# Kernel tuning notes

Hardware: AMD Instinct MI355X
Metric: run time of the kernel (lower is better)

Reference implementation:

```python
import jax, jax.numpy as jnp
import numpy as np
from jax import lax

B, CIN, HID, T, H, W = 4, 32, 32, 31, 96, 96


def setup_inputs() -> dict:
    key = jax.random.key(0)
    k1, k2, k3 = jax.random.split(key, 3)
    inputs = jax.random.normal(k1, (B, CIN, T, H, W), dtype=jnp.float32)
    conv_w = jax.random.normal(k2, (2 * HID, CIN, 3, 3, 3), dtype=jnp.float32) * 0.05
    conv_b = jax.random.normal(k3, (2 * HID,), dtype=jnp.float32) * 0.05
    gamma = jnp.ones((1,), dtype=jnp.float32)
    return {"inputs": inputs, "conv_w": conv_w, "conv_b": conv_b, "gamma": gamma}


def reference(inputs, conv_w, conv_b, gamma):
    hid = conv_w.shape[0] // 2
    # Conv3d, 'same' padding, NCDHW layout -> gates [B, 2*hid, T, H, W]
    gates = lax.conv_general_dilated(
        inputs, conv_w, window_strides=(1, 1, 1), padding="SAME",
        dimension_numbers=("NCDHW", "OIDHW", "NCDHW"))
    gates = gates + conv_b[None, :, None, None, None]
    Z = jnp.tanh(gates[:, :hid])          # [B, hid, T, H, W]
    F = jax.nn.sigmoid(gates[:, hid:])    # [B, hid, T, H, W]

    # Gated recurrence over time (dim 2): h_t = f_t * h_{t-1} + (1 - f_t) * z_t
    Zt = jnp.moveaxis(Z, 2, 0)  # [T, B, hid, H, W]
    Ft = jnp.moveaxis(F, 2, 0)

    def step(h, zf):
        z, f = zf
        h = f * h + (1.0 - f) * z
        return h, h

    h0 = jnp.zeros_like(Zt[0])  # h=None <=> h0=0 since f*0+(1-f)*z
    _, hs = lax.scan(step, h0, (Zt, Ft))
    h_time = jnp.moveaxis(hs, 0, 2)  # [B, hid, T, H, W]

    # Per-spatial-location channel attention
    qh = jnp.transpose(h_time, (0, 3, 4, 1, 2))  # [B, H, W, C, T]
    scores = jnp.einsum("bhwct,bhwdt->bhwcd", qh, qh)  # [B, H, W, C, C]
    attn = jax.nn.softmax(scores, axis=3)  # softmax over row axis c (dim=3), as in torch
    attn = attn * (1.0 / np.sqrt(qh.shape[-2]))  # divide AFTER softmax by sqrt(C)
    ah = jnp.einsum("bhwcd,bhwdt->bhwct", attn, qh)  # [B, H, W, C, T]
    ah = jnp.transpose(ah, (0, 3, 4, 1, 2))  # [B, C, T, H, W]

    return gamma * ah + h_time
```

## Files before the change

### kernel.cpp

```cpp
#include <hip/hip_runtime.h>
#include <math.h>

#define B_ 4
#define CIN_ 32
#define HID_ 32
#define T_ 31
#define H_ 96
#define W_ 96
#define SP_ (H_*W_)

typedef _Float16 half8 __attribute__((ext_vector_type(8)));
typedef float f32x4 __attribute__((ext_vector_type(4)));
typedef float f32x16 __attribute__((ext_vector_type(16)));

static __device__ inline unsigned int packhh(float a, float b) {
  unsigned short ua = __builtin_bit_cast(unsigned short, (_Float16)a);
  unsigned short ub = __builtin_bit_cast(unsigned short, (_Float16)b);
  return (unsigned int)ua | ((unsigned int)ub << 16);
}

__global__ __launch_bounds__(256) void prep_w_kernel(
    const float* __restrict__ w, _Float16* __restrict__ wr) {
  int idx = blockIdx.x * 256 + threadIdx.x;
  if (idx >= 55296) return;
  int i = idx & 7;
  int lane = (idx >> 3) & 63;
  int rest = idx >> 9;
  int tap = rest % 27;
  int ocg = rest / 27;
  int m = lane & 15;
  int cin = (lane >> 4) * 8 + i;
  int oc = (m & 1) * 32 + ocg * 8 + (m >> 1);
  wr[idx] = (_Float16)(w[(oc * CIN_ + cin) * 27 + tap]);
}

#define PITCH 40
#define SROWS 8
#define SCOLS 18
#define SLICE_HF (SROWS * SCOLS * PITCH)

__global__ __launch_bounds__(256, 2) void conv_rec_mfma(
    const float* __restrict__ in, const _Float16* __restrict__ wr,
    const float* __restrict__ bias, unsigned int* __restrict__ gout) {
  __shared__ _Float16 in_s[4 * SLICE_HF];

  const int tid = threadIdx.x;
  const int tile = blockIdx.x;
  const int b = blockIdx.y;
  const int x0 = (tile % 6) * 16;
  const int y0 = (tile / 6) * 6;
  const int lane = tid & 63;
  const int ocg = tid >> 6;
  const int px = lane & 15;
  const int kq = lane >> 4;

  half8 wreg[27];
  {
    const _Float16* wp = wr + (size_t)ocg * 27 * 512 + lane * 8;
#pragma unroll
    for (int tap = 0; tap < 27; ++tap)
      wreg[tap] = *(const half8*)(wp + tap * 512);
  }

  const int c0 = ocg * 8 + 2 * kq;
  f32x4 bias4;
  bias4[0] = bias[c0];
  bias4[1] = bias[32 + c0];
  bias4[2] = bias[c0 + 1];
  bias4[3] = bias[32 + c0 + 1];

  const int s_xi = tid & 15;
  const int s_q  = tid >> 4;
  const int e_cin = tid & 31;
  const int e_yy  = tid >> 5;
  const int e_gy  = y0 - 1 + e_yy;
  const bool e_ok = ((unsigned)e_gy < (unsigned)H_);

  auto stage_full = [&](int ts) {
    _Float16* dst = in_s + (ts & 3) * SLICE_HF;
    const float* sb = in + ((size_t)(b * CIN_) * T_ + ts) * SP_;
#pragma unroll
    for (int k = 0; k < 16; ++k) {
      int rj = k * 16 + s_q;
      int cin = rj & 31;
      int yy = rj >> 5;
      int gy = y0 - 1 + yy;
      float v = 0.f;
      if ((unsigned)gy < (unsigned)H_)
        v = sb[(size_t)cin * (T_ * SP_) + gy * W_ + x0 + s_xi];
      dst[(yy * SCOLS + s_xi + 1) * PITCH + cin] = (_Float16)v;
    }
    float v0 = 0.f, v1 = 0.f;
    if (e_ok) {
      const float* rb = sb + (size_t)e_cin * (T_ * SP_) + e_gy * W_;
      if (x0 > 0) v0 = rb[x0 - 1];
      if (x0 + 16 < W_) v1 = rb[x0 + 16];
    }
    dst[(e_yy * SCOLS + 0) * PITCH + e_cin] = (_Float16)v0;
    dst[(e_yy * SCOLS + 17) * PITCH + e_cin] = (_Float16)v1;
  };

  {
    uint32_t* dz = (uint32_t*)(in_s + 3 * SLICE_HF);
    for (int e = tid; e < SLICE_HF / 2; e += 256) dz[e] = 0u;
  }
  stage_full(0);
  stage_full(1);
  __syncthreads();

  float h[6][2];
#pragma unroll
  for (int r = 0; r < 6; ++r) { h[r][0] = 0.f; h[r][1] = 0.f; }

  const int pr = ocg * 4 + kq;
  size_t obase = ((size_t)(b * 32 + pr) * T_) * SP_ + y0 * W_ + x0 + px;

  for (int t = 0; t < T_; ++t) {
    const int ts = t + 2;

    float sv[16], ev0 = 0.f, ev1 = 0.f;
    if (ts < T_) {
      const float* sb = in + ((size_t)(b * CIN_) * T_ + ts) * SP_;
#pragma unroll
      for (int k = 0; k < 16; ++k) {
        int rj = k * 16 + s_q;
        int cin = rj & 31;
        int yy = rj >> 5;
        int gy = y0 - 1 + yy;
        sv[k] = 0.f;
        if ((unsigned)gy < (unsigned)H_)
          sv[k] = sb[(size_t)cin * (T_ * SP_) + gy * W_ + x0 + s_xi];
      }
      if (e_ok) {
        const float* rb = sb + (size_t)e_cin * (T_ * SP_) + e_gy * W_;
        if (x0 > 0) ev0 = rb[x0 - 1];
        if (x0 + 16 < W_) ev1 = rb[x0 + 16];
      }
    }

    f32x4 acc[6];
#pragma unroll
    for (int r = 0; r < 6; ++r) acc[r] = bias4;

#pragma unroll
    for (int kd = 0; kd < 3; ++kd) {
      const _Float16* sb2 = in_s + ((t + 3 + kd) & 3) * SLICE_HF;
#pragma unroll
      for (int kw = 0; kw < 3; ++kw) {
        half8 brow[8];
#pragma unroll
        for (int rr = 0; rr < 8; ++rr)
          brow[rr] = *(const half8*)(sb2 + (rr * SCOLS + px + kw) * PITCH + kq * 8);
#pragma unroll
        for (int kh = 0; kh < 3; ++kh) {
          const int tap = kd * 9 + kh * 3 + kw;
#pragma unroll
          for (int r = 0; r < 6; ++r)
            acc[r] = __builtin_amdgcn_mfma_f32_16x16x32_f16(wreg[tap], brow[r + kh], acc[r], 0, 0, 0);
        }
      }
    }

    if (ts < T_) {
      _Float16* dst = in_s + (ts & 3) * SLICE_HF;
#pragma unroll
      for (int k = 0; k < 16; ++k) {
        int rj = k * 16 + s_q;
        int cin = rj & 31;
        int yy = rj >> 5;
        dst[(yy * SCOLS + s_xi + 1) * PITCH + cin] = (_Float16)sv[k];
      }
      dst[(e_yy * SCOLS + 0) * PITCH + e_cin] = (_Float16)ev0;
      dst[(e_yy * SCOLS + 17) * PITCH + e_cin] = (_Float16)ev1;
    } else if (ts == T_) {
      uint32_t* dz = (uint32_t*)(in_s + (ts & 3) * SLICE_HF);
      for (int e = tid; e < SLICE_HF / 2; e += 256) dz[e] = 0u;
    }

#pragma unroll
    for (int r = 0; r < 6; ++r) {
      float z0 = 1.f - 2.f / (1.f + __expf(2.f * acc[r][0]));
      float f0 = 1.f / (1.f + __expf(-acc[r][1]));
      h[r][0] = f0 * h[r][0] + (1.f - f0) * z0;
      float z1 = 1.f - 2.f / (1.f + __expf(2.f * acc[r][2]));
      float f1 = 1.f / (1.f + __expf(-acc[r][3]));
      h[r][1] = f1 * h[r][1] + (1.f - f1) * z1;
      gout[obase + r * W_] = packhh(h[r][0], h[r][1]);
    }
    obase += SP_;
    __syncthreads();
  }
}

#define APIT 40
#define PSTR 1288

__global__ __launch_bounds__(512) void attn_mfma(
    unsigned int* __restrict__ g, const float* __restrict__ gamma) {
  __shared__ _Float16 qh_s[16 * PSTR];
  __shared__ _Float16 qt_s[16 * PSTR];
  __shared__ _Float16 at_s[8 * 32 * APIT];

  const int tid = threadIdx.x;
  const int x0 = blockIdx.x * 16;
  const int y = blockIdx.y;
  const int b = blockIdx.z;
  const int lane = tid & 63;
  const int wv = tid >> 6;
  const float gm = gamma[0];

  for (int e = tid; e < 16 * 16 * 31; e += 512) {
    int xi = e & 15;
    int q = e >> 4;
    int t = q % 31;
    int pr = q / 31;
    unsigned int gw = g[((size_t)(b * 32 + pr) * T_ + t) * SP_ + y * W_ + x0 + xi];
    _Float16 h0 = __builtin_bit_cast(_Float16, (unsigned short)(gw & 0xffff));
    _Float16 h1 = __builtin_bit_cast(_Float16, (unsigned short)(gw >> 16));
    int c0 = 2 * pr;
    qh_s[xi * PSTR + c0 * APIT + t] = h0;
    qh_s[xi * PSTR + (c0 + 1) * APIT + t] = h1;
    qt_s[xi * PSTR + t * APIT + c0] = h0;
    qt_s[xi * PSTR + t * APIT + c0 + 1] = h1;
  }
  qh_s[(tid & 15) * PSTR + (tid >> 4) * APIT + 31] = (_Float16)0.f;
  __syncthreads();

  const int cd = lane & 31;
  const int hi = lane >> 5;

#pragma unroll
  for (int pp = 0; pp < 2; ++pp) {
    const int px = wv * 2 + pp;
    const _Float16* qs = qh_s + px * PSTR;
    const _Float16* qt = qt_s + px * PSTR;
    _Float16* as = at_s + wv * (32 * APIT);

    half8 q0 = *(const half8*)(qs + cd * APIT + hi * 8);
    half8 q1 = *(const half8*)(qs + cd * APIT + hi * 8 + 16);
    f32x16 S = {};
    S = __builtin_amdgcn_mfma_f32_32x32x16_f16(q0, q0, S, 0, 0, 0);
    S = __builtin_amdgcn_mfma_f32_32x32x16_f16(q1, q1, S, 0, 0, 0);

    float mx = S[0];
#pragma unroll
    for (int r = 1; r < 16; ++r) mx = fmaxf(mx, S[r]);
    mx = fmaxf(mx, __shfl_xor(mx, 32));
    float sm = 0.f;
    float ev[16];
#pragma unroll
    for (int r = 0; r < 16; ++r) { ev[r] = __expf(S[r] - mx); sm += ev[r]; }
    sm += __shfl_xor(sm, 32);
    const float sc = 0.17677669529663688f / sm;

#pragma unroll
    for (int r = 0; r < 16; ++r) {
      int c = (r & 3) + 8 * (r >> 2) + 4 * hi;
      as[c * APIT + cd] = (_Float16)(ev[r] * sc);
    }

    half8 a0 = *(const half8*)(as + cd * APIT + hi * 8);
    half8 a1 = *(const half8*)(as + cd * APIT + hi * 8 + 16);
    half8 b0 = *(const half8*)(qt + cd * APIT + hi * 8);
    half8 b1 = *(const half8*)(qt + cd * APIT + hi * 8 + 16);
    f32x16 P = {};
    P = __builtin_amdgcn_mfma_f32_32x32x16_f16(a0, b0, P, 0, 0, 0);
    P = __builtin_amdgcn_mfma_f32_32x32x16_f16(a1, b1, P, 0, 0, 0);

#pragma unroll
    for (int r = 0; r < 16; ++r) {
      int c = (r & 3) + 8 * (r >> 2) + 4 * hi;
      qt_s[px * PSTR + cd * APIT + c] = (_Float16)P[r];
    }
  }
  __syncthreads();

  float* gf = (float*)g;
  for (int e = tid; e < 4 * 992; e += 512) {
    int xi4 = e & 3;
    int q = e >> 2;
    int t = q % 31;
    int c = q / 31;
    float4 rv;
#pragma unroll
    for (int j = 0; j < 4; ++j) {
      int xi = xi4 * 4 + j;
      float ah = (float)qt_s[xi * PSTR + t * APIT + c];
      float hv = (float)qh_s[xi * PSTR + c * APIT + t];
      (&rv.x)[j] = gm * ah + hv;
    }
    *(float4*)&gf[((size_t)(b * HID_ + c) * T_ + t) * SP_ + y * W_ + x0 +
                  xi4 * 4] = rv;
  }
}

extern "C" void kernel_launch(void* const* d_in, const int* in_sizes, int n_in,
                              void* d_out, int out_size, void* d_ws,
                              size_t ws_size, hipStream_t stream) {
  const float* in    = (const float*)d_in[0];
  const float* w     = (const float*)d_in[1];
  const float* bias  = (const float*)d_in[2];
  const float* gamma = (const float*)d_in[3];
  _Float16* wr = (_Float16*)d_ws;

  prep_w_kernel<<<216, 256, 0, stream>>>(w, wr);
  conv_rec_mfma<<<dim3(96, 4), 256, 0, stream>>>(
      in, wr, bias, (unsigned int*)d_out);
  attn_mfma<<<dim3(6, 96, 4), 512, 0, stream>>>(
      (unsigned int*)d_out, gamma);
}
```

Before: 282.8 us.

## Swizzle conv LDS layout, precompute staging offsets, move output stores after barrier

Changes how threads map onto input staging so each thread loads 2 channels (s_q and s_q+16) across 8 rows, with precomputed base offsets in place of per-iteration index math. Adds an XOR swizzle on the channel offset (flip 16 when column bit 3 is set) in both LDS writes and the MFMA operand reads, meant to cut bank conflicts. Output gate stores are now issued after the barrier so they overlap the next step. Risk: the swizzle must match exactly between writer and reader, and 32-bit offsets must not overflow.

```diff
diff --git a/kernel.cpp b/kernel.cpp
--- a/kernel.cpp
+++ b/kernel.cpp
@@ -8,6 +8,7 @@
 #define H_ 96
 #define W_ 96
 #define SP_ (H_*W_)
+#define TSP (T_ * SP_)
 
 typedef _Float16 half8 __attribute__((ext_vector_type(8)));
 typedef float f32x4 __attribute__((ext_vector_type(4)));
@@ -37,7 +38,8 @@
 #define PITCH 40
 #define SROWS 8
 #define SCOLS 18
-#define SLICE_HF (SROWS * SCOLS * PITCH)
+#define RST (SCOLS * PITCH)
+#define SLICE_HF (SROWS * RST)
 
 __global__ __launch_bounds__(256, 2) void conv_rec_mfma(
     const float* __restrict__ in, const _Float16* __restrict__ wr,
@@ -71,33 +73,45 @@
 
   const int s_xi = tid & 15;
   const int s_q  = tid >> 4;
+  const int ibase = s_q * TSP + (y0 - 1) * W_ + x0 + s_xi;
+  const int wxm   = ((s_xi + 1) & 8) ? 1 : 0;
+  const int wbase = (s_xi + 1) * PITCH + s_q;
   const int e_cin = tid & 31;
   const int e_yy  = tid >> 5;
   const int e_gy  = y0 - 1 + e_yy;
   const bool e_ok = ((unsigned)e_gy < (unsigned)H_);
+  const int eoff  = e_cin * TSP + e_gy * W_;
+  const int ew0   = e_yy * RST + 0 * PITCH + e_cin;
+  const int ew1   = e_yy * RST + 17 * PITCH + e_cin;
+  const bool has_l = (x0 > 0), has_r = (x0 + 16 < W_);
+
+  int cs[3];
+#pragma unroll
+  for (int kw = 0; kw < 3; ++kw) {
+    int c = px + kw;
+    cs[kw] = c * PITCH + ((kq * 8) ^ ((c & 8) ? 16 : 0));
+  }
+
+  const float* inb = in + (size_t)(b * CIN_) * TSP;
 
   auto stage_full = [&](int ts) {
     _Float16* dst = in_s + (ts & 3) * SLICE_HF;
-    const float* sb = in + ((size_t)(b * CIN_) * T_ + ts) * SP_;
+    const int tso = ts * SP_;
 #pragma unroll
     for (int k = 0; k < 16; ++k) {
-      int rj = k * 16 + s_q;
-      int cin = rj & 31;
-      int yy = rj >> 5;
-      int gy = y0 - 1 + yy;
+      const int gy = y0 - 1 + (k >> 1);
       float v = 0.f;
       if ((unsigned)gy < (unsigned)H_)
-        v = sb[(size_t)cin * (T_ * SP_) + gy * W_ + x0 + s_xi];
-      dst[(yy * SCOLS + s_xi + 1) * PITCH + cin] = (_Float16)v;
+        v = inb[ibase + (k & 1) * 16 * TSP + (k >> 1) * W_ + tso];
+      dst[wbase + (k >> 1) * RST + (((k & 1) ^ wxm) * 16)] = (_Float16)v;
     }
     float v0 = 0.f, v1 = 0.f;
     if (e_ok) {
-      const float* rb = sb + (size_t)e_cin * (T_ * SP_) + e_gy * W_;
-      if (x0 > 0) v0 = rb[x0 - 1];
-      if (x0 + 16 < W_) v1 = rb[x0 + 16];
-    }
-    dst[(e_yy * SCOLS + 0) * PITCH + e_cin] = (_Float16)v0;
-    dst[(e_yy * SCOLS + 17) * PITCH + e_cin] = (_Float16)v1;
+      if (has_l) v0 = inb[eoff + tso + x0 - 1];
+      if (has_r) v1 = inb[eoff + tso + x0 + 16];
+    }
+    dst[ew0] = (_Float16)v0;
+    dst[ew1] = (_Float16)v1;
   };
 
   {
@@ -120,21 +134,17 @@
 
     float sv[16], ev0 = 0.f, ev1 = 0.f;
     if (ts < T_) {
-      const float* sb = in + ((size_t)(b * CIN_) * T_ + ts) * SP_;
+      const int tso = ts * SP_;
 #pragma unroll
       for (int k = 0; k < 16; ++k) {
-        int rj = k * 16 + s_q;
-        int cin = rj & 31;
-        int yy = rj >> 5;
-        int gy = y0 - 1 + yy;
+        const int gy = y0 - 1 + (k >> 1);
         sv[k] = 0.f;
         if ((unsigned)gy < (unsigned)H_)
-          sv[k] = sb[(size_t)cin * (T_ * SP_) + gy * W_ + x0 + s_xi];
+          sv[k] = inb[ibase + (k & 1) * 16 * TSP + (k >> 1) * W_ + tso];
       }
       if (e_ok) {
-        const float* rb = sb + (size_t)e_cin * (T_ * SP_) + e_gy * W_;
-        if (x0 > 0) ev0 = rb[x0 - 1];
-        if (x0 + 16 < W_) ev1 = rb[x0 + 16];
+        if (has_l) ev0 = inb[eoff + tso + x0 - 1];
+        if (has_r) ev1 = inb[eoff + tso + x0 + 16];
       }
     }
 
@@ -150,7 +160,7 @@
         half8 brow[8];
 #pragma unroll
         for (int rr = 0; rr < 8; ++rr)
-          brow[rr] = *(const half8*)(sb2 + (rr * SCOLS + px + kw) * PITCH + kq * 8);
+          brow[rr] = *(const half8*)(sb2 + rr * RST + cs[kw]);
 #pragma unroll
         for (int kh = 0; kh < 3; ++kh) {
           const int tap = kd * 9 + kh * 3 + kw;
@@ -164,19 +174,16 @@
     if (ts < T_) {
       _Float16* dst = in_s + (ts & 3) * SLICE_HF;
 #pragma unroll
-      for (int k = 0; k < 16; ++k) {
-        int rj = k * 16 + s_q;
-        int cin = rj & 31;
-        int yy = rj >> 5;
-        dst[(yy * SCOLS + s_xi + 1) * PITCH + cin] = (_Float16)sv[k];
-      }
-      dst[(e_yy * SCOLS + 0) * PITCH + e_cin] = (_Float16)ev0;
-      dst[(e_yy * SCOLS + 17) * PITCH + e_cin] = (_Float16)ev1;
+      for (int k = 0; k < 16; ++k)
+        dst[wbase + (k >> 1) * RST + (((k & 1) ^ wxm) * 16)] = (_Float16)sv[k];
+      dst[ew0] = (_Float16)ev0;
+      dst[ew1] = (_Float16)ev1;
     } else if (ts == T_) {
       uint32_t* dz = (uint32_t*)(in_s + (ts & 3) * SLICE_HF);
       for (int e = tid; e < SLICE_HF / 2; e += 256) dz[e] = 0u;
     }
 
+    unsigned int pk[6];
 #pragma unroll
     for (int r = 0; r < 6; ++r) {
       float z0 = 1.f - 2.f / (1.f + __expf(2.f * acc[r][0]));
@@ -185,10 +192,14 @@
       float z1 = 1.f - 2.f / (1.f + __expf(2.f * acc[r][2]));
       float f1 = 1.f / (1.f + __expf(-acc[r][3]));
       h[r][1] = f1 * h[r][1] + (1.f - f1) * z1;
-      gout[obase + r * W_] = packhh(h[r][0], h[r][1]);
-    }
+      pk[r] = packhh(h[r][0], h[r][1]);
+    }
+    __syncthreads();
+
+#pragma unroll
+    for (int r = 0; r < 6; ++r)
+      gout[obase + r * W_] = pk[r];
     obase += SP_;
-    __syncthreads();
   }
 }
 
```

Measured after the change: 277.8 us. About the same (-1.8%).

## Halve conv waves so each wave computes two output-channel groups per B-fragment load

Applied to the files above, without the earlier changes.

The conv+recurrence kernel now runs 128 threads (2 waves) per block instead of 256, and each wave holds weights for two output-channel groups. Every LDS B-fragment load therefore feeds two MFMAs, halving LDS read traffic per MFMA. Global stores are moved after the barrier. In exchange, register pressure doubles (54 half8 weight registers), each thread does twice the staging loads, and the grid has only 384 blocks of 2 waves, which lowers occupancy and latency hiding.

```diff
diff --git a/kernel.cpp b/kernel.cpp
--- a/kernel.cpp
+++ b/kernel.cpp
@@ -8,6 +8,7 @@
 #define H_ 96
 #define W_ 96
 #define SP_ (H_*W_)
+#define TSP (T_ * SP_)
 
 typedef _Float16 half8 __attribute__((ext_vector_type(8)));
 typedef float f32x4 __attribute__((ext_vector_type(4)));
@@ -37,9 +38,10 @@
 #define PITCH 40
 #define SROWS 8
 #define SCOLS 18
-#define SLICE_HF (SROWS * SCOLS * PITCH)
-
-__global__ __launch_bounds__(256, 2) void conv_rec_mfma(
+#define RST (SCOLS * PITCH)
+#define SLICE_HF (SROWS * RST)
+
+__global__ __launch_bounds__(128, 1) void conv_rec_mfma(
     const float* __restrict__ in, const _Float16* __restrict__ wr,
     const float* __restrict__ bias, unsigned int* __restrict__ gout) {
   __shared__ _Float16 in_s[4 * SLICE_HF];
@@ -50,97 +52,117 @@
   const int x0 = (tile % 6) * 16;
   const int y0 = (tile / 6) * 6;
   const int lane = tid & 63;
-  const int ocg = tid >> 6;
+  const int wv = tid >> 6;
   const int px = lane & 15;
   const int kq = lane >> 4;
 
-  half8 wreg[27];
+  half8 wA[27], wB[27];
   {
-    const _Float16* wp = wr + (size_t)ocg * 27 * 512 + lane * 8;
-#pragma unroll
-    for (int tap = 0; tap < 27; ++tap)
-      wreg[tap] = *(const half8*)(wp + tap * 512);
-  }
-
-  const int c0 = ocg * 8 + 2 * kq;
-  f32x4 bias4;
-  bias4[0] = bias[c0];
-  bias4[1] = bias[32 + c0];
-  bias4[2] = bias[c0 + 1];
-  bias4[3] = bias[32 + c0 + 1];
+    const _Float16* pa = wr + (size_t)(2 * wv) * 27 * 512 + lane * 8;
+    const _Float16* pb = wr + (size_t)(2 * wv + 1) * 27 * 512 + lane * 8;
+#pragma unroll
+    for (int tap = 0; tap < 27; ++tap) {
+      wA[tap] = *(const half8*)(pa + tap * 512);
+      wB[tap] = *(const half8*)(pb + tap * 512);
+    }
+  }
+
+  const int cA = 16 * wv + 2 * kq;
+  const int cB = cA + 8;
+  f32x4 biasA, biasB;
+  biasA[0] = bias[cA];      biasA[1] = bias[32 + cA];
+  biasA[2] = bias[cA + 1];  biasA[3] = bias[32 + cA + 1];
+  biasB[0] = bias[cB];      biasB[1] = bias[32 + cB];
+  biasB[2] = bias[cB + 1];  biasB[3] = bias[32 + cB + 1];
 
   const int s_xi = tid & 15;
   const int s_q  = tid >> 4;
   const int e_cin = tid & 31;
-  const int e_yy  = tid >> 5;
-  const int e_gy  = y0 - 1 + e_yy;
-  const bool e_ok = ((unsigned)e_gy < (unsigned)H_);
+  const int e_y4  = tid >> 5;
+  const bool has_l = (x0 > 0), has_r = (x0 + 16 < W_);
+
+  const float* inb = in + (size_t)(b * CIN_) * TSP;
 
   auto stage_full = [&](int ts) {
     _Float16* dst = in_s + (ts & 3) * SLICE_HF;
-    const float* sb = in + ((size_t)(b * CIN_) * T_ + ts) * SP_;
-#pragma unroll
-    for (int k = 0; k < 16; ++k) {
-      int rj = k * 16 + s_q;
+    const int tso = ts * SP_;
+#pragma unroll
+    for (int k = 0; k < 32; ++k) {
+      int rj = k * 8 + s_q;
       int cin = rj & 31;
       int yy = rj >> 5;
       int gy = y0 - 1 + yy;
       float v = 0.f;
       if ((unsigned)gy < (unsigned)H_)
-        v = sb[(size_t)cin * (T_ * SP_) + gy * W_ + x0 + s_xi];
+        v = inb[(size_t)cin * TSP + tso + gy * W_ + x0 + s_xi];
       dst[(yy * SCOLS + s_xi + 1) * PITCH + cin] = (_Float16)v;
     }
-    float v0 = 0.f, v1 = 0.f;
-    if (e_ok) {
-      const float* rb = sb + (size_t)e_cin * (T_ * SP_) + e_gy * W_;
-      if (x0 > 0) v0 = rb[x0 - 1];
-      if (x0 + 16 < W_) v1 = rb[x0 + 16];
-    }
-    dst[(e_yy * SCOLS + 0) * PITCH + e_cin] = (_Float16)v0;
-    dst[(e_yy * SCOLS + 17) * PITCH + e_cin] = (_Float16)v1;
+#pragma unroll
+    for (int j = 0; j < 2; ++j) {
+      int yy = e_y4 + 4 * j;
+      int gy = y0 - 1 + yy;
+      float vl = 0.f, vr = 0.f;
+      if ((unsigned)gy < (unsigned)H_) {
+        const float* rb = inb + (size_t)e_cin * TSP + tso + gy * W_;
+        if (has_l) vl = rb[x0 - 1];
+        if (has_r) vr = rb[x0 + 16];
+      }
+      dst[(yy * SCOLS + 0) * PITCH + e_cin] = (_Float16)vl;
+      dst[(yy * SCOLS + 17) * PITCH + e_cin] = (_Float16)vr;
+    }
   };
 
   {
     uint32_t* dz = (uint32_t*)(in_s + 3 * SLICE_HF);
-    for (int e = tid; e < SLICE_HF / 2; e += 256) dz[e] = 0u;
+    for (int e = tid; e < SLICE_HF / 2; e += 128) dz[e] = 0u;
   }
   stage_full(0);
   stage_full(1);
   __syncthreads();
 
-  float h[6][2];
-#pragma unroll
-  for (int r = 0; r < 6; ++r) { h[r][0] = 0.f; h[r][1] = 0.f; }
-
-  const int pr = ocg * 4 + kq;
-  size_t obase = ((size_t)(b * 32 + pr) * T_) * SP_ + y0 * W_ + x0 + px;
+  float h[2][6][2];
+#pragma unroll
+  for (int f = 0; f < 2; ++f)
+#pragma unroll
+    for (int r = 0; r < 6; ++r) { h[f][r][0] = 0.f; h[f][r][1] = 0.f; }
+
+  size_t obA = ((size_t)(b * 32 + 8 * wv + kq) * T_) * SP_ + y0 * W_ + x0 + px;
+  size_t obB = obA + (size_t)4 * TSP;
+
+  int cs[3];
+#pragma unroll
+  for (int kw = 0; kw < 3; ++kw) cs[kw] = (px + kw) * PITCH + kq * 8;
 
   for (int t = 0; t < T_; ++t) {
     const int ts = t + 2;
 
-    float sv[16], ev0 = 0.f, ev1 = 0.f;
+    float sv[32], el[2] = {0.f, 0.f}, er[2] = {0.f, 0.f};
     if (ts < T_) {
-      const float* sb = in + ((size_t)(b * CIN_) * T_ + ts) * SP_;
-#pragma unroll
-      for (int k = 0; k < 16; ++k) {
-        int rj = k * 16 + s_q;
+      const int tso = ts * SP_;
+#pragma unroll
+      for (int k = 0; k < 32; ++k) {
+        int rj = k * 8 + s_q;
         int cin = rj & 31;
         int yy = rj >> 5;
         int gy = y0 - 1 + yy;
         sv[k] = 0.f;
         if ((unsigned)gy < (unsigned)H_)
-          sv[k] = sb[(size_t)cin * (T_ * SP_) + gy * W_ + x0 + s_xi];
-      }
-      if (e_ok) {
-        const float* rb = sb + (size_t)e_cin * (T_ * SP_) + e_gy * W_;
-        if (x0 > 0) ev0 = rb[x0 - 1];
-        if (x0 + 16 < W_) ev1 = rb[x0 + 16];
-      }
-    }
-
-    f32x4 acc[6];
-#pragma unroll
-    for (int r = 0; r < 6; ++r) acc[r] = bias4;
+          sv[k] = inb[(size_t)cin * TSP + tso + gy * W_ + x0 + s_xi];
+      }
+#pragma unroll
+      for (int j = 0; j < 2; ++j) {
+        int gy = y0 - 1 + e_y4 + 4 * j;
+        if ((unsigned)gy < (unsigned)H_) {
+          const float* rb = inb + (size_t)e_cin * TSP + tso + gy * W_;
+          if (has_l) el[j] = rb[x0 - 1];
+          if (has_r) er[j] = rb[x0 + 16];
+        }
+      }
+    }
+
+    f32x4 accA[6], accB[6];
+#pragma unroll
+    for (int r = 0; r < 6; ++r) { accA[r] = biasA; accB[r] = biasB; }
 
 #pragma unroll
     for (int kd = 0; kd < 3; ++kd) {
@@ -150,13 +172,15 @@
         half8 brow[8];
 #pragma unroll
         for (int rr = 0; rr < 8; ++rr)
-          brow[rr] = *(const half8*)(sb2 + (rr * SCOLS + px + kw) * PITCH + kq * 8);
+          brow[rr] = *(const half8*)(sb2 + rr * RST + cs[kw]);
 #pragma unroll
         for (int kh = 0; kh < 3; ++kh) {
           const int tap = kd * 9 + kh * 3 + kw;
 #pragma unroll
-          for (int r = 0; r < 6; ++r)
-            acc[r] = __builtin_amdgcn_mfma_f32_16x16x32_f16(wreg[tap], brow[r + kh], acc[r], 0, 0, 0);
+          for (int r = 0; r < 6; ++r) {
+            accA[r] = __builtin_amdgcn_mfma_f32_16x16x32_f16(wA[tap], brow[r + kh], accA[r], 0, 0, 0);
+            accB[r] = __builtin_amdgcn_mfma_f32_16x16x32_f16(wB[tap], brow[r + kh], accB[r], 0, 0, 0);
+          }
         }
       }
     }
@@ -164,31 +188,50 @@
     if (ts < T_) {
       _Float16* dst = in_s + (ts & 3) * SLICE_HF;
 #pragma unroll
-      for (int k = 0; k < 16; ++k) {
-        int rj = k * 16 + s_q;
+      for (int k = 0; k < 32; ++k) {
+        int rj = k * 8 + s_q;
         int cin = rj & 31;
         int yy = rj >> 5;
         dst[(yy * SCOLS + s_xi + 1) * PITCH + cin] = (_Float16)sv[k];
       }
-      dst[(e_yy * SCOLS + 0) * PITCH + e_cin] = (_Float16)ev0;
-      dst[(e_yy * SCOLS + 17) * PITCH + e_cin] = (_Float16)ev1;
+#pragma unroll
+      for (int j = 0; j < 2; ++j) {
+        int yy = e_y4 + 4 * j;
+        dst[(yy * SCOLS + 0) * PITCH + e_cin] = (_Float16)el[j];
+        dst[(yy * SCOLS + 17) * PITCH + e_cin] = (_Float16)er[j];
+      }
     } else if (ts == T_) {
       uint32_t* dz = (uint32_t*)(in_s + (ts & 3) * SLICE_HF);
-      for (int e = tid; e < SLICE_HF / 2; e += 256) dz[e] = 0u;
-    }
-
+      for (int e = tid; e < SLICE_HF / 2; e += 128) dz[e] = 0u;
+    }
+
+    unsigned int pkA[6], pkB[6];
 #pragma unroll
     for (int r = 0; r < 6; ++r) {
-      float z0 = 1.f - 2.f / (1.f + __expf(2.f * acc[r][0]));
-      float f0 = 1.f / (1.f + __expf(-acc[r][1]));
-      h[r][0] = f0 * h[r][0] + (1.f - f0) * z0;
-      float z1 = 1.f - 2.f / (1.f + __expf(2.f * acc[r][2]));
-      float f1 = 1.f / (1.f + __expf(-acc[r][3]));
-      h[r][1] = f1 * h[r][1] + (1.f - f1) * z1;
-      gout[obase + r * W_] = packhh(h[r][0], h[r][1]);
-    }
-    obase += SP_;
+      float z0 = 1.f - 2.f / (1.f + __expf(2.f * accA[r][0]));
+      float f0 = 1.f / (1.f + __expf(-accA[r][1]));
+      h[0][r][0] = f0 * h[0][r][0] + (1.f - f0) * z0;
+      float z1 = 1.f - 2.f / (1.f + __expf(2.f * accA[r][2]));
+      float f1 = 1.f / (1.f + __expf(-accA[r][3]));
+      h[0][r][1] = f1 * h[0][r][1] + (1.f - f1) * z1;
+      pkA[r] = packhh(h[0][r][0], h[0][r][1]);
+      float z2 = 1.f - 2.f / (1.f + __expf(2.f * accB[r][0]));
+      float f2 = 1.f / (1.f + __expf(-accB[r][1]));
+      h[1][r][0] = f2 * h[1][r][0] + (1.f - f2) * z2;
+      float z3 = 1.f - 2.f / (1.f + __expf(2.f * accB[r][2]));
+      float f3 = 1.f / (1.f + __expf(-accB[r][3]));
+      h[1][r][1] = f3 * h[1][r][1] + (1.f - f3) * z3;
+      pkB[r] = packhh(h[1][r][0], h[1][r][1]);
+    }
     __syncthreads();
+
+#pragma unroll
+    for (int r = 0; r < 6; ++r) {
+      gout[obA + r * W_] = pkA[r];
+      gout[obB + r * W_] = pkB[r];
+    }
+    obA += SP_;
+    obB += SP_;
   }
 }
 
@@ -304,7 +347,7 @@
   _Float16* wr = (_Float16*)d_ws;
 
   prep_w_kernel<<<216, 256, 0, stream>>>(w, wr);
-  conv_rec_mfma<<<dim3(96, 4), 256, 0, stream>>>(
+  conv_rec_mfma<<<dim3(96, 4), 128, 0, stream>>>(
       in, wr, bias, (unsigned int*)d_out);
   attn_mfma<<<dim3(6, 96, 4), 512, 0, stream>>>(
       (unsigned int*)d_out, gamma);
```

After: 304.0 us. 7.5% more time.

## Split conv-recurrence block into two wave groups processing alternating time steps

Applied to the files above, without the earlier changes.

The conv+recurrence kernel doubles its block to 512 threads, with two 256-thread groups each computing the convolution for alternating time steps (t and t+1) from a 6-slot LDS ring. The recurrent hidden state moves from registers into a shared fp16 buffer, handed from group 0 to group 1 across two barriers per pair of steps. The aim is to double the MFMA work in flight per tile and hide load latency, given the grid has only 384 blocks. The cost is extra LDS use and barriers, and the hidden state is now rounded to fp16 between every step, which slightly changes numerics.

```diff
diff --git a/kernel.cpp b/kernel.cpp
--- a/kernel.cpp
+++ b/kernel.cpp
@@ -8,6 +8,7 @@
 #define H_ 96
 #define W_ 96
 #define SP_ (H_*W_)
+#define TSP (T_ * SP_)
 
 typedef _Float16 half8 __attribute__((ext_vector_type(8)));
 typedef float f32x4 __attribute__((ext_vector_type(4)));
@@ -37,20 +38,25 @@
 #define PITCH 40
 #define SROWS 8
 #define SCOLS 18
-#define SLICE_HF (SROWS * SCOLS * PITCH)
-
-__global__ __launch_bounds__(256, 2) void conv_rec_mfma(
+#define RST (SCOLS * PITCH)
+#define SLICE_HF (SROWS * RST)
+#define SLOT(s) ((((s) % 6) + 6) % 6)
+
+__global__ __launch_bounds__(512, 4) void conv_rec_mfma(
     const float* __restrict__ in, const _Float16* __restrict__ wr,
     const float* __restrict__ bias, unsigned int* __restrict__ gout) {
-  __shared__ _Float16 in_s[4 * SLICE_HF];
+  __shared__ _Float16 in_s[6 * SLICE_HF];
+  __shared__ unsigned int hx_s[16 * 96];
 
   const int tid = threadIdx.x;
   const int tile = blockIdx.x;
   const int b = blockIdx.y;
   const int x0 = (tile % 6) * 16;
   const int y0 = (tile / 6) * 6;
+  const int grp = tid >> 8;
+  const int gt  = tid & 255;
   const int lane = tid & 63;
-  const int ocg = tid >> 6;
+  const int ocg = (tid >> 6) & 3;
   const int px = lane & 15;
   const int kq = lane >> 4;
 
@@ -69,16 +75,19 @@
   bias4[2] = bias[c0 + 1];
   bias4[3] = bias[32 + c0 + 1];
 
-  const int s_xi = tid & 15;
-  const int s_q  = tid >> 4;
-  const int e_cin = tid & 31;
-  const int e_yy  = tid >> 5;
+  const int s_xi = gt & 15;
+  const int s_q  = gt >> 4;
+  const int e_cin = gt & 31;
+  const int e_yy  = gt >> 5;
   const int e_gy  = y0 - 1 + e_yy;
   const bool e_ok = ((unsigned)e_gy < (unsigned)H_);
-
-  auto stage_full = [&](int ts) {
-    _Float16* dst = in_s + (ts & 3) * SLICE_HF;
-    const float* sb = in + ((size_t)(b * CIN_) * T_ + ts) * SP_;
+  const bool has_l = (x0 > 0), has_r = (x0 + 16 < W_);
+
+  const float* inb = in + (size_t)(b * CIN_) * TSP;
+
+  auto stage_g = [&](int ts) {
+    _Float16* dst = in_s + SLOT(ts) * SLICE_HF;
+    const int tso = ts * SP_;
 #pragma unroll
     for (int k = 0; k < 16; ++k) {
       int rj = k * 16 + s_q;
@@ -87,40 +96,47 @@
       int gy = y0 - 1 + yy;
       float v = 0.f;
       if ((unsigned)gy < (unsigned)H_)
-        v = sb[(size_t)cin * (T_ * SP_) + gy * W_ + x0 + s_xi];
+        v = inb[(size_t)cin * TSP + tso + gy * W_ + x0 + s_xi];
       dst[(yy * SCOLS + s_xi + 1) * PITCH + cin] = (_Float16)v;
     }
     float v0 = 0.f, v1 = 0.f;
     if (e_ok) {
-      const float* rb = sb + (size_t)e_cin * (T_ * SP_) + e_gy * W_;
-      if (x0 > 0) v0 = rb[x0 - 1];
-      if (x0 + 16 < W_) v1 = rb[x0 + 16];
+      const float* rb = inb + (size_t)e_cin * TSP + tso + e_gy * W_;
+      if (has_l) v0 = rb[x0 - 1];
+      if (has_r) v1 = rb[x0 + 16];
     }
     dst[(e_yy * SCOLS + 0) * PITCH + e_cin] = (_Float16)v0;
     dst[(e_yy * SCOLS + 17) * PITCH + e_cin] = (_Float16)v1;
   };
 
   {
-    uint32_t* dz = (uint32_t*)(in_s + 3 * SLICE_HF);
-    for (int e = tid; e < SLICE_HF / 2; e += 256) dz[e] = 0u;
-  }
-  stage_full(0);
-  stage_full(1);
+    uint32_t* dz = (uint32_t*)(in_s + 5 * SLICE_HF);
+    for (int e = tid; e < SLICE_HF / 2; e += 512) dz[e] = 0u;
+    for (int e = tid; e < 16 * 96; e += 512) hx_s[e] = 0u;
+  }
+  if (grp == 0) stage_g(0); else stage_g(1);
+  if (grp == 0) stage_g(2);
   __syncthreads();
 
-  float h[6][2];
-#pragma unroll
-  for (int r = 0; r < 6; ++r) { h[r][0] = 0.f; h[r][1] = 0.f; }
-
   const int pr = ocg * 4 + kq;
-  size_t obase = ((size_t)(b * 32 + pr) * T_) * SP_ + y0 * W_ + x0 + px;
-
-  for (int t = 0; t < T_; ++t) {
-    const int ts = t + 2;
+  const int hxb = pr * 96 + px;
+  size_t obase = ((size_t)(b * 32 + pr) * T_ + grp) * SP_ + y0 * W_ + x0 + px;
+
+  int cs[3];
+#pragma unroll
+  for (int kw = 0; kw < 3; ++kw) cs[kw] = (px + kw) * PITCH + kq * 8;
+
+  for (int p = 0; p < 16; ++p) {
+    const int t0 = 2 * p;
+    const int tm = t0 + grp;
+    const int ts = t0 + 3 + grp;
+    const bool do_conv = (tm < T_);
+    const bool do_stage = (ts < T_);
+    const bool do_zero  = (ts == T_);
 
     float sv[16], ev0 = 0.f, ev1 = 0.f;
-    if (ts < T_) {
-      const float* sb = in + ((size_t)(b * CIN_) * T_ + ts) * SP_;
+    if (do_stage) {
+      const int tso = ts * SP_;
 #pragma unroll
       for (int k = 0; k < 16; ++k) {
         int rj = k * 16 + s_q;
@@ -129,40 +145,42 @@
         int gy = y0 - 1 + yy;
         sv[k] = 0.f;
         if ((unsigned)gy < (unsigned)H_)
-          sv[k] = sb[(size_t)cin * (T_ * SP_) + gy * W_ + x0 + s_xi];
+          sv[k] = inb[(size_t)cin * TSP + tso + gy * W_ + x0 + s_xi];
       }
       if (e_ok) {
-        const float* rb = sb + (size_t)e_cin * (T_ * SP_) + e_gy * W_;
-        if (x0 > 0) ev0 = rb[x0 - 1];
-        if (x0 + 16 < W_) ev1 = rb[x0 + 16];
+        const float* rb = inb + (size_t)e_cin * TSP + tso + e_gy * W_;
+        if (has_l) ev0 = rb[x0 - 1];
+        if (has_r) ev1 = rb[x0 + 16];
       }
     }
 
     f32x4 acc[6];
 #pragma unroll
     for (int r = 0; r < 6; ++r) acc[r] = bias4;
-
-#pragma unroll
-    for (int kd = 0; kd < 3; ++kd) {
-      const _Float16* sb2 = in_s + ((t + 3 + kd) & 3) * SLICE_HF;
-#pragma unroll
-      for (int kw = 0; kw < 3; ++kw) {
-        half8 brow[8];
-#pragma unroll
-        for (int rr = 0; rr < 8; ++rr)
-          brow[rr] = *(const half8*)(sb2 + (rr * SCOLS + px + kw) * PITCH + kq * 8);
-#pragma unroll
-        for (int kh = 0; kh < 3; ++kh) {
-          const int tap = kd * 9 + kh * 3 + kw;
-#pragma unroll
-          for (int r = 0; r < 6; ++r)
-            acc[r] = __builtin_amdgcn_mfma_f32_16x16x32_f16(wreg[tap], brow[r + kh], acc[r], 0, 0, 0);
+    if (do_conv) {
+#pragma unroll
+      for (int kd = 0; kd < 3; ++kd) {
+        const _Float16* sb2 = in_s + SLOT(tm - 1 + kd) * SLICE_HF;
+#pragma unroll
+        for (int kw = 0; kw < 3; ++kw) {
+          half8 brow[8];
+#pragma unroll
+          for (int rr = 0; rr < 8; ++rr)
+            brow[rr] = *(const half8*)(sb2 + rr * RST + cs[kw]);
+#pragma unroll
+          for (int kh = 0; kh < 3; ++kh) {
+            const int tap = kd * 9 + kh * 3 + kw;
+#pragma unroll
+            for (int r = 0; r < 6; ++r)
+              acc[r] = __builtin_amdgcn_mfma_f32_16x16x32_f16(
+                  wreg[tap], brow[r + kh], acc[r], 0, 0, 0);
+          }
         }
       }
     }
 
-    if (ts < T_) {
-      _Float16* dst = in_s + (ts & 3) * SLICE_HF;
+    if (do_stage) {
+      _Float16* dst = in_s + SLOT(ts) * SLICE_HF;
 #pragma unroll
       for (int k = 0; k < 16; ++k) {
         int rj = k * 16 + s_q;
@@ -172,23 +190,56 @@
       }
       dst[(e_yy * SCOLS + 0) * PITCH + e_cin] = (_Float16)ev0;
       dst[(e_yy * SCOLS + 17) * PITCH + e_cin] = (_Float16)ev1;
-    } else if (ts == T_) {
-      uint32_t* dz = (uint32_t*)(in_s + (ts & 3) * SLICE_HF);
-      for (int e = tid; e < SLICE_HF / 2; e += 256) dz[e] = 0u;
-    }
-
-#pragma unroll
-    for (int r = 0; r < 6; ++r) {
-      float z0 = 1.f - 2.f / (1.f + __expf(2.f * acc[r][0]));
-      float f0 = 1.f / (1.f + __expf(-acc[r][1]));
-      h[r][0] = f0 * h[r][0] + (1.f - f0) * z0;
-      float z1 = 1.f - 2.f / (1.f + __expf(2.f * acc[r][2]));
-      float f1 = 1.f / (1.f + __expf(-acc[r][3]));
-      h[r][1] = f1 * h[r][1] + (1.f - f1) * z1;
-      gout[obase + r * W_] = packhh(h[r][0], h[r][1]);
-    }
-    obase += SP_;
+    } else if (do_zero) {
+      uint32_t* dz = (uint32_t*)(in_s + SLOT(T_) * SLICE_HF);
+      for (int e = gt; e < SLICE_HF / 2; e += 256) dz[e] = 0u;
+    }
+
+    unsigned int pk[6];
+    bool stv = false;
+    if (grp == 0) {
+#pragma unroll
+      for (int r = 0; r < 6; ++r) {
+        unsigned int old = hx_s[hxb + r * 16];
+        float h0 = (float)__builtin_bit_cast(_Float16, (unsigned short)(old & 0xffff));
+        float h1 = (float)__builtin_bit_cast(_Float16, (unsigned short)(old >> 16));
+        float z0 = 1.f - 2.f / (1.f + __expf(2.f * acc[r][0]));
+        float f0 = 1.f / (1.f + __expf(-acc[r][1]));
+        h0 = f0 * (h0 - z0) + z0;
+        float z1 = 1.f - 2.f / (1.f + __expf(2.f * acc[r][2]));
+        float f1 = 1.f / (1.f + __expf(-acc[r][3]));
+        h1 = f1 * (h1 - z1) + z1;
+        pk[r] = packhh(h0, h1);
+        hx_s[hxb + r * 16] = pk[r];
+      }
+      stv = true;
+    }
     __syncthreads();
+
+    if (grp == 1 && do_conv) {
+#pragma unroll
+      for (int r = 0; r < 6; ++r) {
+        unsigned int old = hx_s[hxb + r * 16];
+        float h0 = (float)__builtin_bit_cast(_Float16, (unsigned short)(old & 0xffff));
+        float h1 = (float)__builtin_bit_cast(_Float16, (unsigned short)(old >> 16));
+        float z0 = 1.f - 2.f / (1.f + __expf(2.f * acc[r][0]));
+        float f0 = 1.f / (1.f + __expf(-acc[r][1]));
+        h0 = f0 * (h0 - z0) + z0;
+        float z1 = 1.f - 2.f / (1.f + __expf(2.f * acc[r][2]));
+        float f1 = 1.f / (1.f + __expf(-acc[r][3]));
+        h1 = f1 * (h1 - z1) + z1;
+        pk[r] = packhh(h0, h1);
+        hx_s[hxb + r * 16] = pk[r];
+      }
+      stv = true;
+    }
+    __syncthreads();
+
+    if (stv) {
+#pragma unroll
+      for (int r = 0; r < 6; ++r) gout[obase + r * W_] = pk[r];
+    }
+    obase += 2 * SP_;
   }
 }
 
@@ -304,7 +355,7 @@
   _Float16* wr = (_Float16*)d_ws;
 
   prep_w_kernel<<<216, 256, 0, stream>>>(w, wr);
-  conv_rec_mfma<<<dim3(96, 4), 256, 0, stream>>>(
+  conv_rec_mfma<<<dim3(96, 4), 512, 0, stream>>>(
       in, wr, bias, (unsigned int*)d_out);
   attn_mfma<<<dim3(6, 96, 4), 512, 0, stream>>>(
       (unsigned int*)d_out, gamma);
```

After: 405.0 us. 43.2% more time.
